# Performance work log

Measured on AMD Instinct MI355X. Metric: run time of the kernel, lower is better.

## Reference

```python
import jax, jax.numpy as jnp
import numpy as np

B, T, H, L = 8, 256, 64, 3
NB, NF, HP = 17, 68, 6
K = 9  # temporal kernel
PAD = (K - 1) // 2
EPS = 1e-5


def _normalize(adj):
    adj = adj + np.eye(adj.shape[0], dtype=np.float32)
    d = adj.sum(1)
    dinv = np.power(d, -0.5)
    dinv[np.isinf(dinv)] = 0.0
    return (dinv[:, None] * adj * dinv[None, :]).astype(np.float32)


def _body_adj():
    a = np.zeros((NB, NB), np.float32)
    conns = [(0, 1), (0, 2), (1, 3), (2, 4), (0, 5), (0, 6), (5, 6), (5, 7), (7, 9), (6, 8), (8, 10), (5, 11), (6, 12), (11, 12), (11, 13), (13, 15), (12, 14), (14, 16)]
    for i, j in conns:
        a[i, j] = 1.0
        a[j, i] = 1.0
    return _normalize(a)


def _face_adj():
    a = np.zeros((NF, NF), np.float32)
    for i in range(16): a[i, i + 1] = 1.0
    for i in range(17, 21): a[i, i + 1] = 1.0
    for i in range(22, 26): a[i, i + 1] = 1.0
    for i in range(27, 30): a[i, i + 1] = 1.0
    for i in range(31, 35): a[i, i + 1] = 1.0
    for i in range(36, 41): a[i, i + 1] = 1.0
    a[41, 36] = 1.0
    for i in range(42, 47): a[i, i + 1] = 1.0
    a[47, 42] = 1.0
    for i in range(48, 59): a[i, i + 1] = 1.0
    a[59, 48] = 1.0
    for i in range(60, 67): a[i, i + 1] = 1.0
    a[67, 60] = 1.0
    a = a + a.T
    return _normalize(a)


def setup_inputs() -> dict:
    keys = iter(jax.random.split(jax.random.key(0), 80))

    def rn(shape, s):
        return jax.random.normal(next(keys), shape, jnp.float32) * s

    inp = {}
    inp['body_kps'] = jax.random.normal(next(keys), (B, T, NB * 2), jnp.float32)
    inp['face_kps_2d'] = jax.random.normal(next(keys), (B, T, NF * 2), jnp.float32)
    inp['head_pose'] = jax.random.normal(next(keys), (B, T, HP), jnp.float32)
    inp['body_adj'] = jnp.asarray(_body_adj())
    inp['face_adj'] = jnp.asarray(_face_adj())
    inp['body_proj_w'] = rn((2, H), 0.5)
    inp['body_proj_b'] = jnp.zeros((H,), jnp.float32)
    inp['face_proj_w'] = rn((2, H), 0.5)
    inp['face_proj_b'] = jnp.zeros((H,), jnp.float32)
    inp['head_w'] = rn((HP, H), 0.3)
    inp['head_b'] = jnp.zeros((H,), jnp.float32)
    for p in ('b', 'f'):
        inp[p + '_t1w'] = rn((L, H, H, K), 0.04)
        inp[p + '_t1b'] = jnp.zeros((L, H), jnp.float32)
        inp[p + '_bn1g'] = jnp.ones((L, H), jnp.float32)
        inp[p + '_bn1b'] = jnp.zeros((L, H), jnp.float32)
        inp[p + '_bn1m'] = rn((L, H), 0.1)
        inp[p + '_bn1v'] = jax.random.uniform(next(keys), (L, H), jnp.float32, 0.5, 1.5)
        inp[p + '_gcw'] = rn((L, H, H), 0.1)
        inp[p + '_gcb'] = jnp.zeros((L, H), jnp.float32)
        inp[p + '_t2w'] = rn((L, H, H, K), 0.04)
        inp[p + '_t2b'] = jnp.zeros((L, H), jnp.float32)
        inp[p + '_bn2g'] = jnp.ones((L, H), jnp.float32)
        inp[p + '_bn2b'] = jnp.zeros((L, H), jnp.float32)
        inp[p + '_bn2m'] = rn((L, H), 0.1)
        inp[p + '_bn2v'] = jax.random.uniform(next(keys), (L, H), jnp.float32, 0.5, 1.5)
    total = NB * H + NF * H + H  # 5504
    inp['fus1_w'] = rn((total, 4 * H), 0.02)
    inp['fus1_b'] = jnp.zeros((4 * H,), jnp.float32)
    inp['fus2_w'] = rn((4 * H, 2 * H), 0.06)
    inp['fus2_b'] = jnp.zeros((2 * H,), jnp.float32)
    inp['fus3_w'] = rn((2 * H, H), 0.09)
    inp['fus3_b'] = jnp.zeros((H,), jnp.float32)
    inp['fus4_w'] = rn((H, 5), 0.12)
    inp['fus4_b'] = jnp.zeros((5,), jnp.float32)
    return inp


def _conv_bn(x, w, b, g, be, m, v):
    # x: (BN, C, T); w: (O, I, K). Conv1d (pad=4) + eval-mode BatchNorm1d.
    y = jax.lax.conv_general_dilated(x, w, (1,), [(PAD, PAD)], dimension_numbers=('NCH', 'OIH', 'NCH'))
    y = y + b[None, :, None]
    inv = g * jax.lax.rsqrt(v + EPS)
    return y * inv[None, :, None] + (be - m * inv)[None, :, None]


def _block(x, adj, t1w, t1b, g1, b1, m1, v1, gw, gb, t2w, t2b, g2, b2, m2, v2):
    # x: (B, N, C, T); residual is identity (in_channels == out_channels)
    Bn, N, C, Tn = x.shape
    res = x
    h = jax.nn.relu(_conv_bn(x.reshape(Bn * N, C, Tn), t1w, t1b, g1, b1, m1, v1)).reshape(Bn, N, C, Tn)
    # spatial graph conv, batched over all timesteps at once (adj @ (x W) + b)
    support = jnp.einsum('bnct,co->bnot', h, gw)
    h = jax.nn.relu(jnp.einsum('mn,bnot->bmot', adj, support) + gb[None, None, :, None])
    h = _conv_bn(h.reshape(Bn * N, C, Tn), t2w, t2b, g2, b2, m2, v2).reshape(Bn, N, C, Tn)
    return h + res  # dropout = identity in eval


def _stream(x, n_nodes, pw, pb, adj, ps):
    Bn, Tn, _ = x.shape
    h = x.reshape(Bn, Tn, n_nodes, 2) @ pw + pb          # (B, T, N, H)
    h = jnp.transpose(h, (0, 2, 3, 1))                   # (B, N, H, T)
    for l in range(ps[0].shape[0]):
        h = _block(h, adj, *(p[l] for p in ps))
    return h.mean(axis=3).reshape(Bn, -1)                # temporal mean-pool, flatten nodes


def reference(body_kps, face_kps_2d, head_pose, body_adj, face_adj, body_proj_w, body_proj_b, face_proj_w, face_proj_b, head_w, head_b, b_t1w, b_t1b, b_bn1g, b_bn1b, b_bn1m, b_bn1v, b_gcw, b_gcb, b_t2w, b_t2b, b_bn2g, b_bn2b, b_bn2m, b_bn2v, f_t1w, f_t1b, f_bn1g, f_bn1b, f_bn1m, f_bn1v, f_gcw, f_gcb, f_t2w, f_t2b, f_bn2g, f_bn2b, f_bn2m, f_bn2v, fus1_w, fus1_b, fus2_w, fus2_b, fus3_w, fus3_b, fus4_w, fus4_b):
    bps = (b_t1w, b_t1b, b_bn1g, b_bn1b, b_bn1m, b_bn1v, b_gcw, b_gcb, b_t2w, b_t2b, b_bn2g, b_bn2b, b_bn2m, b_bn2v)
    fps = (f_t1w, f_t1b, f_bn1g, f_bn1b, f_bn1m, f_bn1v, f_gcw, f_gcb, f_t2w, f_t2b, f_bn2g, f_bn2b, f_bn2m, f_bn2v)
    bf = _stream(body_kps, NB, body_proj_w, body_proj_b, body_adj, bps)
    ff = _stream(face_kps_2d, NF, face_proj_w, face_proj_b, face_adj, fps)
    hp = jax.nn.relu(head_pose @ head_w + head_b).mean(axis=1)
    feat = jnp.concatenate([bf, ff, hp], axis=-1)
    h = jax.nn.relu(feat @ fus1_w + fus1_b)
    h = jax.nn.relu(h @ fus2_w + fus2_b)
    h = jax.nn.relu(h @ fus3_w + fus3_b)
    return h @ fus4_w + fus4_b
```

## Files before the change

kernel.cpp:

```cpp
#include <hip/hip_runtime.h>

constexpr int B_ = 8, T_ = 256, H_ = 64, L_ = 3, NB_ = 17, NF_ = 68, HP_ = 6, K_ = 9;
constexpr int FEAT_DIM = NB_ * H_ + NF_ * H_ + H_;
constexpr int HT = H_ * T_;

typedef _Float16 half4_t __attribute__((ext_vector_type(4)));
typedef _Float16 half8_t __attribute__((ext_vector_type(8)));
typedef float f32x16 __attribute__((ext_vector_type(16)));
typedef float f32x4 __attribute__((ext_vector_type(4)));

constexpr size_t SZ_AB = (size_t)B_ * NB_ * HT;
constexpr size_t SZ_AF = (size_t)B_ * NF_ * HT;
constexpr size_t OFF_TB   = 0;
constexpr size_t OFF_TF   = OFF_TB + SZ_AB / 2;
constexpr size_t OFF_SUPB = OFF_TF + SZ_AF / 2;
constexpr size_t OFF_SUPF = OFF_SUPB + SZ_AB / 2;
constexpr size_t OFF_GB   = OFF_SUPF + SZ_AF / 2;
constexpr size_t OFF_GF   = OFF_GB + SZ_AB / 2;
constexpr size_t OFF_W3   = OFF_GF + SZ_AF / 2;
constexpr size_t OFF_GW3  = OFF_W3 + 4 * 55296;
constexpr size_t OFF_B2   = OFF_GW3 + 2 * 6144;
constexpr size_t OFF_ADJPB= OFF_B2 + 768;
constexpr size_t OFF_ADJPF= OFF_ADJPB + 512;
constexpr size_t OFF_FEAT = OFF_ADJPF + 3840;
constexpr size_t OFF_P1   = OFF_FEAT + (size_t)B_ * FEAT_DIM;

struct ConvPrepSet { const float *w, *tb, *g, *bb, *m, *v; };

struct Args {
    const float *body_kps, *face_kps, *head_pose, *body_adj, *face_adj;
    const float *body_pw, *body_pb, *face_pw, *face_pb, *head_w, *head_b;
    ConvPrepSet sb1, sb2, sf1, sf2;
    const float *b_gcw, *f_gcw, *b_gcb, *f_gcb;
    const float *fus1_w, *fus1_b, *fus2_w, *fus2_b, *fus3_w, *fus3_b, *fus4_w, *fus4_b;
    _Float16 *TrB, *TrF, *SupB, *SupF, *Gb, *Gf;
    _Float16 *W3, *GW3, *adjPB, *adjPF;
    float *B2, *p1, *feat;
    float *out;
};

__device__ __forceinline__ half8_t ld_b8(const _Float16* p) {
    half4_t lo = *(const half4_t*)p;
    half4_t hi = *(const half4_t*)(p + 4);
    return __builtin_shufflevector(lo, hi, 0, 1, 2, 3, 4, 5, 6, 7);
}

__device__ __forceinline__ void st_b8(_Float16* p, half8_t v) {
    half4_t lo, hi;
#pragma unroll
    for (int j = 0; j < 4; ++j) { lo[j] = v[j]; hi[j] = v[4 + j]; }
    *(half4_t*)p = lo;
    *(half4_t*)(p + 4) = hi;
}

__device__ __forceinline__ void stage_chunk(const _Float16* __restrict__ xb,
                                            _Float16* __restrict__ Xs, int tc, int tid) {
    for (int u = tid; u < 136 * 8; u += 256) {
        int row = u >> 3, c = u & 7;
        int t = tc * 128 + row - 4;
        half8_t v;
        if (t >= 0 && t < T_) {
            v = *(const half8_t*)(xb + (size_t)t * H_ + c * 8);
        } else {
#pragma unroll
            for (int j = 0; j < 8; ++j) v[j] = (_Float16)0.f;
        }
        st_b8(&Xs[row * 68 + c * 8], v);
    }
}

__device__ __forceinline__ void stage_res_chunk(const _Float16* __restrict__ xb,
                                                _Float16* __restrict__ Rs, int tc, int tid) {
    for (int u = tid; u < 128 * 8; u += 256) {
        int row = u >> 3, c = u & 7;
        half8_t v = *(const half8_t*)(xb + (size_t)(tc * 128 + row) * H_ + c * 8);
        st_b8(&Rs[row * 68 + c * 8], v);
    }
}

__device__ __forceinline__ void conv_kloop(const half8_t* __restrict__ wl,
                                           const _Float16* __restrict__ Xs,
                                           int trow, int ln31, int kg,
                                           f32x16 (&acc)[2]) {
    const _Float16* xr0 = Xs + (size_t)(trow + ln31) * 68;
#pragma unroll
    for (int tap = 0; tap < K_; ++tap) {
#pragma unroll
        for (int ks = 0; ks < 4; ++ks) {
            int i8 = ks * 2 + kg;
            half8_t a0 = wl[(tap * 8 + i8) * H_ + ln31];
            half8_t a1 = wl[(tap * 8 + i8) * H_ + 32 + ln31];
            half8_t bf = ld_b8(xr0 + tap * 68 + i8 * 8);
            acc[0] = __builtin_amdgcn_mfma_f32_32x32x16_f16(a0, bf, acc[0], 0, 0, 0);
            acc[1] = __builtin_amdgcn_mfma_f32_32x32x16_f16(a1, bf, acc[1], 0, 0, 0);
        }
    }
}

__device__ void convmix_core(const half8_t* __restrict__ wl,
                             const float* __restrict__ b1l,
                             const half8_t* __restrict__ gl,
                             _Float16* __restrict__ supb,
                             int tc, _Float16* __restrict__ Xs, int tid) {
    int ln = tid & 63;
    int w = __builtin_amdgcn_readfirstlane(tid >> 6);
    int ln31 = ln & 31, kg = ln >> 5;
    int trow = w * 32;

    f32x16 acc[2];
#pragma unroll
    for (int mt = 0; mt < 2; ++mt)
#pragma unroll
        for (int r = 0; r < 16; ++r) acc[mt][r] = 0.f;

    conv_kloop(wl, Xs, trow, ln31, kg, acc);
    __syncthreads();

    _Float16* mrow = Xs + (size_t)(4 + trow + ln31) * 68;
#pragma unroll
    for (int mt = 0; mt < 2; ++mt) {
#pragma unroll
        for (int rg = 0; rg < 4; ++rg) {
            int o0 = mt * 32 + rg * 8 + kg * 4;
            f32x4 bv = *(const f32x4*)(b1l + o0);
            half4_t hv;
#pragma unroll
            for (int j = 0; j < 4; ++j)
                hv[j] = (_Float16)fmaxf(acc[mt][rg * 4 + j] + bv[j], 0.f);
            *(half4_t*)(mrow + o0) = hv;
        }
    }
    __syncthreads();

    f32x16 acc2[2];
#pragma unroll
    for (int mt = 0; mt < 2; ++mt)
#pragma unroll
        for (int r = 0; r < 16; ++r) acc2[mt][r] = 0.f;
#pragma unroll
    for (int ks = 0; ks < 4; ++ks) {
        int i8 = ks * 2 + kg;
        half8_t a0 = gl[i8 * H_ + ln31];
        half8_t a1 = gl[i8 * H_ + 32 + ln31];
        half8_t b0 = ld_b8(mrow + i8 * 8);
        acc2[0] = __builtin_amdgcn_mfma_f32_32x32x16_f16(a0, b0, acc2[0], 0, 0, 0);
        acc2[1] = __builtin_amdgcn_mfma_f32_32x32x16_f16(a1, b0, acc2[1], 0, 0, 0);
    }

#pragma unroll
    for (int mt = 0; mt < 2; ++mt) {
#pragma unroll
        for (int rg = 0; rg < 4; ++rg) {
            int o0 = mt * 32 + rg * 8 + kg * 4;
            half4_t hv;
#pragma unroll
            for (int j = 0; j < 4; ++j)
                hv[j] = (_Float16)acc2[mt][rg * 4 + j];
            *(half4_t*)(mrow + o0) = hv;
        }
    }
    __syncthreads();
    _Float16* gout = supb + (size_t)(tc * 128) * H_;
    const _Float16* srow = Xs + 4 * 68;
#pragma unroll
    for (int k2 = 0; k2 < 4; ++k2) {
        int u = k2 * 256 + tid;
        int r = u >> 3, c = u & 7;
        half8_t v = ld_b8(srow + r * 68 + c * 8);
        *(half8_t*)(gout + (size_t)r * H_ + c * 8) = v;
    }
}

__global__ __launch_bounds__(256) void prep_k(Args A) {
    int blk = blockIdx.x;
    int tid = threadIdx.x;
    if (blk < 1728) {
        int set = blk / 432;
        int bx = blk % 432;
        ConvPrepSet s = (set == 0) ? A.sb1 : (set == 1) ? A.sb2 : (set == 2) ? A.sf1 : A.sf2;
        int idx = bx * 256 + tid;
        int k = idx % K_; int r = idx / K_;
        int i = r % H_; r /= H_;
        int o = r % H_; int l = r / H_;
        float sc = s.g[l * H_ + o] * rsqrtf(s.v[l * H_ + o] + 1e-5f);
        A.W3[(size_t)set * 110592 + ((((l * K_ + k) * 8 + (i >> 3)) * H_ + o) * 8) + (i & 7)]
            = (_Float16)(s.w[idx] * sc);
        if (i == 0 && k == 0)
            A.B2[set * 192 + l * H_ + o] =
                s.tb[l * H_ + o] * sc + s.bb[l * H_ + o] - s.m[l * H_ + o] * sc;
    } else if (blk < 1824) {
        int set = (blk - 1728) / 48;
        int bx = (blk - 1728) % 48;
        const float* gw = set ? A.f_gcw : A.b_gcw;
        int idx = bx * 256 + tid;
        int o = idx % H_; int r = idx / H_;
        int c = r % H_; int l = r / H_;
        A.GW3[(size_t)set * 12288 + (((l * 8 + (c >> 3)) * H_ + o) * 8) + (c & 7)]
            = (_Float16)gw[idx];
    } else {
        int idx = (blk - 1824) * 256 + tid;
        if (idx < 1024) {
            int m = idx >> 5, k = idx & 31;
            A.adjPB[idx] = (m < NB_ && k < NB_) ? (_Float16)A.body_adj[m * NB_ + k] : (_Float16)0.f;
        } else if (idx < 8704) {
            int j = idx - 1024;
            int m = j / 80, k = j % 80;
            A.adjPF[j] = (m < NF_ && k < NF_) ? (_Float16)A.face_adj[m * NF_ + k] : (_Float16)0.f;
        } else if (idx < 10752) {
            A.p1[idx - 8704] = 0.f;
        } else if (idx < 10752 + B_ * FEAT_DIM) {
            A.feat[idx - 10752] = 0.f;
        }
    }
}

__global__ __launch_bounds__(256, 4) void projcm_k(Args A) {
    __shared__ __align__(16) _Float16 Xs[136 * 68];
    int blk = blockIdx.x, tid = threadIdx.x;
    bool isB = blk < 2 * B_ * NB_;
    int j = isB ? blk : blk - 2 * B_ * NB_;
    int bn = j >> 1, tc = j & 1;
    const float* kps = isB ? A.body_kps : A.face_kps;
    const float* pw  = isB ? A.body_pw  : A.face_pw;
    const float* pb  = isB ? A.body_pb  : A.face_pb;
    _Float16* trunk  = isB ? A.TrB : A.TrF;
    int N = isB ? NB_ : NF_;
    int b = bn / N, n = bn % N;

    for (int u = tid; u < 272; u += 256) {
        int row = u >> 1, hf = u & 1;
        int t = tc * 128 + row - 4;
        _Float16* xr = Xs + row * 68 + hf * 32;
        if (t >= 0 && t < T_) {
            float x0 = kps[((size_t)b * T_ + t) * (N * 2) + n * 2 + 0];
            float x1 = kps[((size_t)b * T_ + t) * (N * 2) + n * 2 + 1];
            bool own = (row >= 4 && row < 132);
            _Float16* ob = trunk + (size_t)bn * HT + (size_t)t * H_ + hf * 32;
#pragma unroll
            for (int cg2 = 0; cg2 < 4; ++cg2) {
                half8_t v;
#pragma unroll
                for (int jj = 0; jj < 8; ++jj) {
                    int c = hf * 32 + cg2 * 8 + jj;
                    v[jj] = (_Float16)fmaf(x0, pw[c], fmaf(x1, pw[H_ + c], pb[c]));
                }
                st_b8(xr + cg2 * 8, v);
                if (own) *(half8_t*)(ob + cg2 * 8) = v;
            }
        } else {
            half8_t z;
#pragma unroll
            for (int jj = 0; jj < 8; ++jj) z[jj] = (_Float16)0.f;
            st_b8(xr, z);
            st_b8(xr + 8, z);
            st_b8(xr + 16, z);
            st_b8(xr + 24, z);
        }
    }
    __syncthreads();

    const half8_t* w1 = (const half8_t*)(A.W3 + (isB ? 0 : 221184));
    const float* b1l  = isB ? A.B2 : A.B2 + 384;
    const half8_t* gl = (const half8_t*)(A.GW3 + (isB ? 0 : 12288));
    _Float16* supb = (isB ? A.SupB : A.SupF) + (size_t)bn * HT;
    convmix_core(w1, b1l, gl, supb, tc, Xs, tid);
}

__global__ __launch_bounds__(256, 4) void cm_k(Args A, int l) {
    __shared__ __align__(16) _Float16 Xs[136 * 68];
    int blk = blockIdx.x, tid = threadIdx.x;
    bool isB = blk < 2 * B_ * NB_;
    int j = isB ? blk : blk - 2 * B_ * NB_;
    int bn = j >> 1, tc = j & 1;
    const _Float16* trunk = isB ? A.TrB : A.TrF;

    stage_chunk(trunk + (size_t)bn * HT, Xs, tc, tid);
    __syncthreads();

    const half8_t* w1 = (const half8_t*)(A.W3 + (isB ? 0 : 221184)) + (size_t)l * (K_ * 8 * H_);
    const float* b1l  = (isB ? A.B2 : A.B2 + 384) + l * H_;
    const half8_t* gl = (const half8_t*)(A.GW3 + (isB ? 0 : 12288)) + (size_t)l * (8 * H_);
    _Float16* supb = (isB ? A.SupB : A.SupF) + (size_t)bn * HT;
    convmix_core(w1, b1l, gl, supb, tc, Xs, tid);
}

template <int N, int MT, int KS>
__device__ void adjmix_impl(const _Float16* __restrict__ sup,
                            const half8_t* __restrict__ adjP,
                            const float* __restrict__ gb,
                            _Float16* __restrict__ out,
                            int blk, int l, _Float16* Ls, int tid) {
    constexpr int KP = KS * 16;
    constexpr int PITCH = KP + 4;
    int b = blk >> 7, cb = blk & 127;
    int colbase = cb * 128;

    for (int u = tid; u < KP * 16; u += 256) {
        int n = u >> 4, cs = u & 15;
        half8_t v;
        if (n < N) v = *(const half8_t*)(sup + (size_t)(b * N + n) * HT + colbase + cs * 8);
        else {
#pragma unroll
            for (int j = 0; j < 8; ++j) v[j] = (_Float16)0.f;
        }
#pragma unroll
        for (int j = 0; j < 8; ++j) Ls[(cs * 8 + j) * PITCH + n] = v[j];
    }
    __syncthreads();

    int ln = tid & 63;
    int w = __builtin_amdgcn_readfirstlane(tid >> 6);
    int ln31 = ln & 31, kg = ln >> 5;
    int colL = w * 32 + ln31;

    f32x16 acc[MT];
#pragma unroll
    for (int mt = 0; mt < MT; ++mt)
#pragma unroll
        for (int r = 0; r < 16; ++r) acc[mt][r] = 0.f;

#pragma unroll
    for (int ks = 0; ks < KS; ++ks) {
        half8_t bf = ld_b8(&Ls[colL * PITCH + ks * 16 + kg * 8]);
#pragma unroll
        for (int mt = 0; mt < MT; ++mt) {
            half8_t af = adjP[(size_t)(mt * 32 + ln31) * (KP / 8) + ks * 2 + kg];
            acc[mt] = __builtin_amdgcn_mfma_f32_32x32x16_f16(af, bf, acc[mt], 0, 0, 0);
        }
    }
    __syncthreads();

    float gbv = gb[l * H_ + (colL & 63)];
#pragma unroll
    for (int mt = 0; mt < MT; ++mt) {
#pragma unroll
        for (int r = 0; r < 16; ++r) {
            int m = mt * 32 + (r & 3) + 8 * (r >> 2) + 4 * kg;
            Ls[m * 132 + colL] = (_Float16)fmaxf(acc[mt][r] + gbv, 0.f);
        }
    }
    __syncthreads();

    for (int u = tid; u < N * 16; u += 256) {
        int m = u >> 4, c = u & 15;
        half8_t v = ld_b8(&Ls[m * 132 + c * 8]);
        *(half8_t*)(out + (size_t)(b * N + m) * HT + colbase + c * 8) = v;
    }
}

__global__ __launch_bounds__(256) void adjmix_k(Args A, int l) {
    __shared__ __align__(16) _Float16 Ls[12800];
    int blk = blockIdx.x, tid = threadIdx.x;
    if (blk < 1024)
        adjmix_impl<NB_, 1, 2>(A.SupB, (const half8_t*)A.adjPB, A.b_gcb, A.Gb, blk, l, Ls, tid);
    else
        adjmix_impl<NF_, 3, 5>(A.SupF, (const half8_t*)A.adjPF, A.f_gcb, A.Gf, blk - 1024, l, Ls, tid);
}

__global__ __launch_bounds__(256, 4) void c2_k(Args A, int l) {
    __shared__ __align__(16) _Float16 Xs[136 * 68];
    __shared__ __align__(16) _Float16 Rs[128 * 68];
    int blk = blockIdx.x, tid = threadIdx.x;
    bool isB = blk < 2 * B_ * NB_;
    int j = isB ? blk : blk - 2 * B_ * NB_;
    int bn = j >> 1, tc = j & 1;
    const _Float16* G = isB ? A.Gb : A.Gf;
    _Float16* trunk   = isB ? A.TrB : A.TrF;
    const half8_t* w2 = (const half8_t*)(A.W3 + (isB ? 110592 : 331776)) + (size_t)l * (K_ * 8 * H_);
    const float* b2l  = (isB ? A.B2 + 192 : A.B2 + 576) + l * H_;

    stage_chunk(G + (size_t)bn * HT, Xs, tc, tid);
    stage_res_chunk(trunk + (size_t)bn * HT, Rs, tc, tid);
    __syncthreads();

    int ln = tid & 63;
    int w = __builtin_amdgcn_readfirstlane(tid >> 6);
    int ln31 = ln & 31, kg = ln >> 5;
    int trow = w * 32;

    f32x16 acc[2];
#pragma unroll
    for (int mt = 0; mt < 2; ++mt)
#pragma unroll
        for (int r = 0; r < 16; ++r) acc[mt][r] = 0.f;

    conv_kloop(w2, Xs, trow, ln31, kg, acc);
    __syncthreads();

    {
        _Float16* orow = Xs + (size_t)(4 + trow + ln31) * 68;
        const _Float16* rrow = Rs + (size_t)(trow + ln31) * 68;
#pragma unroll
        for (int mt = 0; mt < 2; ++mt) {
#pragma unroll
            for (int rg = 0; rg < 4; ++rg) {
                int o0 = mt * 32 + rg * 8 + kg * 4;
                f32x4 bv = *(const f32x4*)(b2l + o0);
                half4_t rv = *(const half4_t*)(rrow + o0);
                half4_t hv;
#pragma unroll
                for (int jj = 0; jj < 4; ++jj)
                    hv[jj] = (_Float16)(acc[mt][rg * 4 + jj] + bv[jj] + (float)rv[jj]);
                *(half4_t*)(orow + o0) = hv;
            }
        }
    }
    __syncthreads();

    _Float16* gout = trunk + (size_t)bn * HT + (size_t)(tc * 128) * H_;
    const _Float16* srow = Xs + 4 * 68;
#pragma unroll
    for (int k2 = 0; k2 < 4; ++k2) {
        int u = k2 * 256 + tid;
        int r = u >> 3, c = u & 7;
        half8_t v = ld_b8(srow + r * 68 + c * 8);
        *(half8_t*)(gout + (size_t)r * H_ + c * 8) = v;
    }
}

__global__ __launch_bounds__(256, 4) void c2last_k(Args A) {
    __shared__ __align__(16) _Float16 Xs[136 * 68];
    __shared__ __align__(16) _Float16 Rs[128 * 68];
    int blk = blockIdx.x, tid = threadIdx.x;
    if (blk >= 1360) {
        int b = blk - 1360;
        if (tid < 64) {
            int c = tid;
            float w0 = A.head_w[c], w1 = A.head_w[64 + c], w2 = A.head_w[128 + c],
                  w3 = A.head_w[192 + c], w4 = A.head_w[256 + c], w5 = A.head_w[320 + c];
            float bias = A.head_b[c];
            float acc = 0.f;
            for (int t = 0; t < T_; ++t) {
                const float* xr = A.head_pose + ((size_t)b * T_ + t) * HP_;
                float s = fmaf(xr[0], w0, fmaf(xr[1], w1, fmaf(xr[2], w2,
                          fmaf(xr[3], w3, fmaf(xr[4], w4, fmaf(xr[5], w5, bias))))));
                acc += fmaxf(s, 0.f);
            }
            A.feat[(size_t)b * FEAT_DIM + NB_ * H_ + NF_ * H_ + c] = acc * (1.f / 256.f);
        }
        return;
    }
    constexpr int l = L_ - 1;
    bool isB = blk < 2 * B_ * NB_;
    int j = isB ? blk : blk - 2 * B_ * NB_;
    int bn = j >> 1, tc = j & 1;
    const _Float16* G = isB ? A.Gb : A.Gf;
    _Float16* trunk   = isB ? A.TrB : A.TrF;
    const half8_t* w2 = (const half8_t*)(A.W3 + (isB ? 110592 : 331776)) + (size_t)l * (K_ * 8 * H_);
    const float* b2l  = (isB ? A.B2 + 192 : A.B2 + 576) + l * H_;
    int N = isB ? NB_ : NF_;
    int fbase = isB ? 0 : NB_ * H_;

    stage_chunk(G + (size_t)bn * HT, Xs, tc, tid);
    stage_res_chunk(trunk + (size_t)bn * HT, Rs, tc, tid);
    __syncthreads();

    int ln = tid & 63;
    int w = __builtin_amdgcn_readfirstlane(tid >> 6);
    int ln31 = ln & 31, kg = ln >> 5;
    int trow = w * 32;

    f32x16 acc[2];
#pragma unroll
    for (int mt = 0; mt < 2; ++mt)
#pragma unroll
        for (int r = 0; r < 16; ++r) acc[mt][r] = 0.f;

    conv_kloop(w2, Xs, trow, ln31, kg, acc);

    float sv[2][16];
    const _Float16* rrow = Rs + (size_t)(trow + ln31) * 68;
#pragma unroll
    for (int mt = 0; mt < 2; ++mt) {
#pragma unroll
        for (int rg = 0; rg < 4; ++rg) {
            int o0 = mt * 32 + rg * 8 + kg * 4;
            f32x4 bv = *(const f32x4*)(b2l + o0);
            half4_t rv = *(const half4_t*)(rrow + o0);
#pragma unroll
            for (int jj = 0; jj < 4; ++jj) {
                int r = rg * 4 + jj;
                float s = acc[mt][r] + bv[jj] + (float)rv[jj];
#pragma unroll
                for (int off = 1; off < 32; off <<= 1) s += __shfl_xor(s, off);
                sv[mt][r] = s;
            }
        }
    }
    __syncthreads();
    float* red = (float*)Xs;
    if (ln31 == 0) {
#pragma unroll
        for (int mt = 0; mt < 2; ++mt)
#pragma unroll
            for (int r = 0; r < 16; ++r) {
                int o = mt * 32 + (r & 3) + 8 * (r >> 2) + 4 * kg;
                red[w * 64 + o] = sv[mt][r];
            }
    }
    __syncthreads();
    if (tid < 64) {
        float s = red[tid] + red[64 + tid] + red[128 + tid] + red[192 + tid];
        int b = bn / N, n = bn % N;
        atomicAdd(&A.feat[(size_t)b * FEAT_DIM + fbase + n * H_ + tid], s * (1.f / 256.f));
    }
}

__global__ __launch_bounds__(256) void fus1_k(Args A) {
    __shared__ float fv[8][64];
    int blk = blockIdx.x;
    int ic = blk >> 1, kh = blk & 1;
    int base = ic * 128 + kh * 64;
    int tid = threadIdx.x;
    for (int u = tid; u < 8 * 64; u += 256) {
        int b = u >> 6, j = u & 63;
        fv[b][j] = A.feat[(size_t)b * FEAT_DIM + base + j];
    }
    __syncthreads();
    float acc[8];
#pragma unroll
    for (int b = 0; b < 8; ++b) acc[b] = 0.f;
    const float* wb = A.fus1_w + (size_t)base * 256 + tid;
    for (int i = 0; i < 64; ++i) {
        float wv = wb[(size_t)i * 256];
#pragma unroll
        for (int b = 0; b < 8; ++b) acc[b] = fmaf(fv[b][i], wv, acc[b]);
    }
#pragma unroll
    for (int b = 0; b < 8; ++b) atomicAdd(&A.p1[b * 256 + tid], acc[b]);
}

__global__ __launch_bounds__(256) void fus_tail_k(Args A) {
    __shared__ float s1[256], s2[128], s3[64];
    int b = blockIdx.x, tid = threadIdx.x;
    s1[tid] = fmaxf(A.p1[b * 256 + tid] + A.fus1_b[tid], 0.f);
    __syncthreads();
    if (tid < 128) {
        float acc = A.fus2_b[tid];
        for (int i = 0; i < 256; ++i) acc = fmaf(s1[i], A.fus2_w[i * 128 + tid], acc);
        s2[tid] = fmaxf(acc, 0.f);
    }
    __syncthreads();
    if (tid < 64) {
        float acc = A.fus3_b[tid];
        for (int i = 0; i < 128; ++i) acc = fmaf(s2[i], A.fus3_w[i * 64 + tid], acc);
        s3[tid] = fmaxf(acc, 0.f);
    }
    __syncthreads();
    if (tid < 5) {
        float acc = A.fus4_b[tid];
        for (int i = 0; i < 64; ++i) acc = fmaf(s3[i], A.fus4_w[i * 5 + tid], acc);
        A.out[b * 5 + tid] = acc;
    }
}

extern "C" void kernel_launch(void* const* d_in, const int* in_sizes, int n_in,
                              void* d_out, int out_size, void* d_ws, size_t ws_size,
                              hipStream_t stream) {
    float* ws = (float*)d_ws;

    Args A;
    A.body_kps = (const float*)d_in[0];
    A.face_kps = (const float*)d_in[1];
    A.head_pose = (const float*)d_in[2];
    A.body_adj = (const float*)d_in[3];
    A.face_adj = (const float*)d_in[4];
    A.body_pw = (const float*)d_in[5];
    A.body_pb = (const float*)d_in[6];
    A.face_pw = (const float*)d_in[7];
    A.face_pb = (const float*)d_in[8];
    A.head_w = (const float*)d_in[9];
    A.head_b = (const float*)d_in[10];
    A.sb1 = ConvPrepSet{(const float*)d_in[11], (const float*)d_in[12], (const float*)d_in[13],
                        (const float*)d_in[14], (const float*)d_in[15], (const float*)d_in[16]};
    A.b_gcw = (const float*)d_in[17];
    A.b_gcb = (const float*)d_in[18];
    A.sb2 = ConvPrepSet{(const float*)d_in[19], (const float*)d_in[20], (const float*)d_in[21],
                        (const float*)d_in[22], (const float*)d_in[23], (const float*)d_in[24]};
    A.sf1 = ConvPrepSet{(const float*)d_in[25], (const float*)d_in[26], (const float*)d_in[27],
                        (const float*)d_in[28], (const float*)d_in[29], (const float*)d_in[30]};
    A.f_gcw = (const float*)d_in[31];
    A.f_gcb = (const float*)d_in[32];
    A.sf2 = ConvPrepSet{(const float*)d_in[33], (const float*)d_in[34], (const float*)d_in[35],
                        (const float*)d_in[36], (const float*)d_in[37], (const float*)d_in[38]};
    A.fus1_w = (const float*)d_in[39]; A.fus1_b = (const float*)d_in[40];
    A.fus2_w = (const float*)d_in[41]; A.fus2_b = (const float*)d_in[42];
    A.fus3_w = (const float*)d_in[43]; A.fus3_b = (const float*)d_in[44];
    A.fus4_w = (const float*)d_in[45]; A.fus4_b = (const float*)d_in[46];

    A.TrB  = (_Float16*)(ws + OFF_TB);
    A.TrF  = (_Float16*)(ws + OFF_TF);
    A.SupB = (_Float16*)(ws + OFF_SUPB);
    A.SupF = (_Float16*)(ws + OFF_SUPF);
    A.Gb   = (_Float16*)(ws + OFF_GB);
    A.Gf   = (_Float16*)(ws + OFF_GF);
    A.W3   = (_Float16*)(ws + OFF_W3);
    A.GW3  = (_Float16*)(ws + OFF_GW3);
    A.adjPB= (_Float16*)(ws + OFF_ADJPB);
    A.adjPF= (_Float16*)(ws + OFF_ADJPF);
    A.B2   = ws + OFF_B2;
    A.feat = ws + OFF_FEAT;
    A.p1   = ws + OFF_P1;
    A.out  = (float*)d_out;

    prep_k<<<2038, 256, 0, stream>>>(A);
    projcm_k<<<1360, 256, 0, stream>>>(A);
    for (int l = 0; l < L_; ++l) {
        adjmix_k<<<2048, 256, 0, stream>>>(A, l);
        if (l < L_ - 1) {
            c2_k<<<1360, 256, 0, stream>>>(A, l);
            cm_k<<<1360, 256, 0, stream>>>(A, l + 1);
        } else {
            c2last_k<<<1368, 256, 0, stream>>>(A);
        }
    }
    fus1_k<<<86, 256, 0, stream>>>(A);
    fus_tail_k<<<8, 256, 0, stream>>>(A);
}
```

Measured before the change: 382.9 us.

## Halve temporal tile to 64 rows and split waves across output-channel halves

The conv kernels now process 64-timestep chunks instead of 128, giving four chunks per node sequence and twice as many blocks. Each wave computes one 32x32 output tile, split as 2 time-slices by 2 output-channel halves, instead of two output tiles over 32 timesteps. Shared memory per block shrinks, and the launch bounds request 8 blocks per CU instead of 4, to raise occupancy and balance the grid. The cost is more halo recomputation (8 of 72 rows instead of 8 of 136), more block overhead, and twice as many atomicAdds into the pooled features.

After: 372.8 us (median of 2 runs). 1.03x faster.

```diff
diff --git a/kernel.cpp b/kernel.cpp
--- a/kernel.cpp
+++ b/kernel.cpp
@@ -53,11 +53,11 @@
     *(half4_t*)(p + 4) = hi;
 }
 
-__device__ __forceinline__ void stage_chunk(const _Float16* __restrict__ xb,
-                                            _Float16* __restrict__ Xs, int tc, int tid) {
-    for (int u = tid; u < 136 * 8; u += 256) {
+__device__ __forceinline__ void stage_chunk64(const _Float16* __restrict__ xb,
+                                              _Float16* __restrict__ Xs, int tc, int tid) {
+    for (int u = tid; u < 72 * 8; u += 256) {
         int row = u >> 3, c = u & 7;
-        int t = tc * 128 + row - 4;
+        int t = tc * 64 + row - 4;
         half8_t v;
         if (t >= 0 && t < T_) {
             v = *(const half8_t*)(xb + (size_t)t * H_ + c * 8);
@@ -69,30 +69,28 @@
     }
 }
 
-__device__ __forceinline__ void stage_res_chunk(const _Float16* __restrict__ xb,
-                                                _Float16* __restrict__ Rs, int tc, int tid) {
-    for (int u = tid; u < 128 * 8; u += 256) {
+__device__ __forceinline__ void stage_res64(const _Float16* __restrict__ xb,
+                                            _Float16* __restrict__ Rs, int tc, int tid) {
+    for (int u = tid; u < 64 * 8; u += 256) {
         int row = u >> 3, c = u & 7;
-        half8_t v = *(const half8_t*)(xb + (size_t)(tc * 128 + row) * H_ + c * 8);
+        half8_t v = *(const half8_t*)(xb + (size_t)(tc * 64 + row) * H_ + c * 8);
         st_b8(&Rs[row * 68 + c * 8], v);
     }
 }
 
 __device__ __forceinline__ void conv_kloop(const half8_t* __restrict__ wl,
                                            const _Float16* __restrict__ Xs,
-                                           int trow, int ln31, int kg,
-                                           f32x16 (&acc)[2]) {
+                                           int trow, int ln31, int kg, int ot,
+                                           f32x16& acc) {
     const _Float16* xr0 = Xs + (size_t)(trow + ln31) * 68;
 #pragma unroll
     for (int tap = 0; tap < K_; ++tap) {
 #pragma unroll
         for (int ks = 0; ks < 4; ++ks) {
             int i8 = ks * 2 + kg;
-            half8_t a0 = wl[(tap * 8 + i8) * H_ + ln31];
-            half8_t a1 = wl[(tap * 8 + i8) * H_ + 32 + ln31];
+            half8_t a = wl[(tap * 8 + i8) * H_ + ot * 32 + ln31];
             half8_t bf = ld_b8(xr0 + tap * 68 + i8 * 8);
-            acc[0] = __builtin_amdgcn_mfma_f32_32x32x16_f16(a0, bf, acc[0], 0, 0, 0);
-            acc[1] = __builtin_amdgcn_mfma_f32_32x32x16_f16(a1, bf, acc[1], 0, 0, 0);
+            acc = __builtin_amdgcn_mfma_f32_32x32x16_f16(a, bf, acc, 0, 0, 0);
         }
     }
 }
@@ -105,65 +103,55 @@
     int ln = tid & 63;
     int w = __builtin_amdgcn_readfirstlane(tid >> 6);
     int ln31 = ln & 31, kg = ln >> 5;
-    int trow = w * 32;
-
-    f32x16 acc[2];
-#pragma unroll
-    for (int mt = 0; mt < 2; ++mt)
-#pragma unroll
-        for (int r = 0; r < 16; ++r) acc[mt][r] = 0.f;
-
-    conv_kloop(wl, Xs, trow, ln31, kg, acc);
+    int ts = w & 1, ot = w >> 1;
+    int trow = ts * 32;
+
+    f32x16 acc;
+#pragma unroll
+    for (int r = 0; r < 16; ++r) acc[r] = 0.f;
+
+    conv_kloop(wl, Xs, trow, ln31, kg, ot, acc);
     __syncthreads();
 
     _Float16* mrow = Xs + (size_t)(4 + trow + ln31) * 68;
 #pragma unroll
-    for (int mt = 0; mt < 2; ++mt) {
-#pragma unroll
-        for (int rg = 0; rg < 4; ++rg) {
-            int o0 = mt * 32 + rg * 8 + kg * 4;
-            f32x4 bv = *(const f32x4*)(b1l + o0);
-            half4_t hv;
-#pragma unroll
-            for (int j = 0; j < 4; ++j)
-                hv[j] = (_Float16)fmaxf(acc[mt][rg * 4 + j] + bv[j], 0.f);
-            *(half4_t*)(mrow + o0) = hv;
-        }
-    }
-    __syncthreads();
-
-    f32x16 acc2[2];
-#pragma unroll
-    for (int mt = 0; mt < 2; ++mt)
-#pragma unroll
-        for (int r = 0; r < 16; ++r) acc2[mt][r] = 0.f;
+    for (int rg = 0; rg < 4; ++rg) {
+        int o0 = ot * 32 + rg * 8 + kg * 4;
+        f32x4 bv = *(const f32x4*)(b1l + o0);
+        half4_t hv;
+#pragma unroll
+        for (int j = 0; j < 4; ++j)
+            hv[j] = (_Float16)fmaxf(acc[rg * 4 + j] + bv[j], 0.f);
+        *(half4_t*)(mrow + o0) = hv;
+    }
+    __syncthreads();
+
+    f32x16 acc2;
+#pragma unroll
+    for (int r = 0; r < 16; ++r) acc2[r] = 0.f;
 #pragma unroll
     for (int ks = 0; ks < 4; ++ks) {
         int i8 = ks * 2 + kg;
-        half8_t a0 = gl[i8 * H_ + ln31];
-        half8_t a1 = gl[i8 * H_ + 32 + ln31];
-        half8_t b0 = ld_b8(mrow + i8 * 8);
-        acc2[0] = __builtin_amdgcn_mfma_f32_32x32x16_f16(a0, b0, acc2[0], 0, 0, 0);
-        acc2[1] = __builtin_amdgcn_mfma_f32_32x32x16_f16(a1, b0, acc2[1], 0, 0, 0);
-    }
-
-#pragma unroll
-    for (int mt = 0; mt < 2; ++mt) {
-#pragma unroll
-        for (int rg = 0; rg < 4; ++rg) {
-            int o0 = mt * 32 + rg * 8 + kg * 4;
-            half4_t hv;
-#pragma unroll
-            for (int j = 0; j < 4; ++j)
-                hv[j] = (_Float16)acc2[mt][rg * 4 + j];
-            *(half4_t*)(mrow + o0) = hv;
-        }
-    }
-    __syncthreads();
-    _Float16* gout = supb + (size_t)(tc * 128) * H_;
+        half8_t a = gl[i8 * H_ + ot * 32 + ln31];
+        half8_t bf = ld_b8(mrow + i8 * 8);
+        acc2 = __builtin_amdgcn_mfma_f32_32x32x16_f16(a, bf, acc2, 0, 0, 0);
+    }
+    __syncthreads();
+
+#pragma unroll
+    for (int rg = 0; rg < 4; ++rg) {
+        int o0 = ot * 32 + rg * 8 + kg * 4;
+        half4_t hv;
+#pragma unroll
+        for (int j = 0; j < 4; ++j)
+            hv[j] = (_Float16)acc2[rg * 4 + j];
+        *(half4_t*)(mrow + o0) = hv;
+    }
+    __syncthreads();
+    _Float16* gout = supb + (size_t)(tc * 64) * H_;
     const _Float16* srow = Xs + 4 * 68;
 #pragma unroll
-    for (int k2 = 0; k2 < 4; ++k2) {
+    for (int k2 = 0; k2 < 2; ++k2) {
         int u = k2 * 256 + tid;
         int r = u >> 3, c = u & 7;
         half8_t v = ld_b8(srow + r * 68 + c * 8);
@@ -214,12 +202,12 @@
     }
 }
 
-__global__ __launch_bounds__(256, 4) void projcm_k(Args A) {
-    __shared__ __align__(16) _Float16 Xs[136 * 68];
+__global__ __launch_bounds__(256, 8) void projcm_k(Args A) {
+    __shared__ __align__(16) _Float16 Xs[72 * 68];
     int blk = blockIdx.x, tid = threadIdx.x;
-    bool isB = blk < 2 * B_ * NB_;
-    int j = isB ? blk : blk - 2 * B_ * NB_;
-    int bn = j >> 1, tc = j & 1;
+    bool isB = blk < 4 * B_ * NB_;
+    int j = isB ? blk : blk - 4 * B_ * NB_;
+    int bn = j >> 2, tc = j & 3;
     const float* kps = isB ? A.body_kps : A.face_kps;
     const float* pw  = isB ? A.body_pw  : A.face_pw;
     const float* pb  = isB ? A.body_pb  : A.face_pb;
@@ -227,14 +215,14 @@
     int N = isB ? NB_ : NF_;
     int b = bn / N, n = bn % N;
 
-    for (int u = tid; u < 272; u += 256) {
-        int row = u >> 1, hf = u & 1;
-        int t = tc * 128 + row - 4;
+    if (tid < 144) {
+        int row = tid >> 1, hf = tid & 1;
+        int t = tc * 64 + row - 4;
         _Float16* xr = Xs + row * 68 + hf * 32;
         if (t >= 0 && t < T_) {
             float x0 = kps[((size_t)b * T_ + t) * (N * 2) + n * 2 + 0];
             float x1 = kps[((size_t)b * T_ + t) * (N * 2) + n * 2 + 1];
-            bool own = (row >= 4 && row < 132);
+            bool own = (row >= 4 && row < 68);
             _Float16* ob = trunk + (size_t)bn * HT + (size_t)t * H_ + hf * 32;
 #pragma unroll
             for (int cg2 = 0; cg2 < 4; ++cg2) {
@@ -266,15 +254,15 @@
     convmix_core(w1, b1l, gl, supb, tc, Xs, tid);
 }
 
-__global__ __launch_bounds__(256, 4) void cm_k(Args A, int l) {
-    __shared__ __align__(16) _Float16 Xs[136 * 68];
+__global__ __launch_bounds__(256, 8) void cm_k(Args A, int l) {
+    __shared__ __align__(16) _Float16 Xs[72 * 68];
     int blk = blockIdx.x, tid = threadIdx.x;
-    bool isB = blk < 2 * B_ * NB_;
-    int j = isB ? blk : blk - 2 * B_ * NB_;
-    int bn = j >> 1, tc = j & 1;
+    bool isB = blk < 4 * B_ * NB_;
+    int j = isB ? blk : blk - 4 * B_ * NB_;
+    int bn = j >> 2, tc = j & 3;
     const _Float16* trunk = isB ? A.TrB : A.TrF;
 
-    stage_chunk(trunk + (size_t)bn * HT, Xs, tc, tid);
+    stage_chunk64(trunk + (size_t)bn * HT, Xs, tc, tid);
     __syncthreads();
 
     const half8_t* w1 = (const half8_t*)(A.W3 + (isB ? 0 : 221184)) + (size_t)l * (K_ * 8 * H_);
@@ -357,60 +345,56 @@
         adjmix_impl<NF_, 3, 5>(A.SupF, (const half8_t*)A.adjPF, A.f_gcb, A.Gf, blk - 1024, l, Ls, tid);
 }
 
-__global__ __launch_bounds__(256, 4) void c2_k(Args A, int l) {
-    __shared__ __align__(16) _Float16 Xs[136 * 68];
-    __shared__ __align__(16) _Float16 Rs[128 * 68];
+__global__ __launch_bounds__(256, 8) void c2_k(Args A, int l) {
+    __shared__ __align__(16) _Float16 Xs[72 * 68];
+    __shared__ __align__(16) _Float16 Rs[64 * 68];
     int blk = blockIdx.x, tid = threadIdx.x;
-    bool isB = blk < 2 * B_ * NB_;
-    int j = isB ? blk : blk - 2 * B_ * NB_;
-    int bn = j >> 1, tc = j & 1;
+    bool isB = blk < 4 * B_ * NB_;
+    int j = isB ? blk : blk - 4 * B_ * NB_;
+    int bn = j >> 2, tc = j & 3;
     const _Float16* G = isB ? A.Gb : A.Gf;
     _Float16* trunk   = isB ? A.TrB : A.TrF;
     const half8_t* w2 = (const half8_t*)(A.W3 + (isB ? 110592 : 331776)) + (size_t)l * (K_ * 8 * H_);
     const float* b2l  = (isB ? A.B2 + 192 : A.B2 + 576) + l * H_;
 
-    stage_chunk(G + (size_t)bn * HT, Xs, tc, tid);
-    stage_res_chunk(trunk + (size_t)bn * HT, Rs, tc, tid);
+    stage_chunk64(G + (size_t)bn * HT, Xs, tc, tid);
+    stage_res64(trunk + (size_t)bn * HT, Rs, tc, tid);
     __syncthreads();
 
     int ln = tid & 63;
     int w = __builtin_amdgcn_readfirstlane(tid >> 6);
     int ln31 = ln & 31, kg = ln >> 5;
-    int trow = w * 32;
-
-    f32x16 acc[2];
-#pragma unroll
-    for (int mt = 0; mt < 2; ++mt)
-#pragma unroll
-        for (int r = 0; r < 16; ++r) acc[mt][r] = 0.f;
-
-    conv_kloop(w2, Xs, trow, ln31, kg, acc);
+    int ts = w & 1, ot = w >> 1;
+    int trow = ts * 32;
+
+    f32x16 acc;
+#pragma unroll
+    for (int r = 0; r < 16; ++r) acc[r] = 0.f;
+
+    conv_kloop(w2, Xs, trow, ln31, kg, ot, acc);
     __syncthreads();
 
     {
         _Float16* orow = Xs + (size_t)(4 + trow + ln31) * 68;
         const _Float16* rrow = Rs + (size_t)(trow + ln31) * 68;
 #pragma unroll
-        for (int mt = 0; mt < 2; ++mt) {
-#pragma unroll
-            for (int rg = 0; rg < 4; ++rg) {
-                int o0 = mt * 32 + rg * 8 + kg * 4;
-                f32x4 bv = *(const f32x4*)(b2l + o0);
-                half4_t rv = *(const half4_t*)(rrow + o0);
-                half4_t hv;
-#pragma unroll
-                for (int jj = 0; jj < 4; ++jj)
-                    hv[jj] = (_Float16)(acc[mt][rg * 4 + jj] + bv[jj] + (float)rv[jj]);
-                *(half4_t*)(orow + o0) = hv;
-            }
-        }
-    }
-    __syncthreads();
-
-    _Float16* gout = trunk + (size_t)bn * HT + (size_t)(tc * 128) * H_;
+        for (int rg = 0; rg < 4; ++rg) {
+            int o0 = ot * 32 + rg * 8 + kg * 4;
+            f32x4 bv = *(const f32x4*)(b2l + o0);
+            half4_t rv = *(const half4_t*)(rrow + o0);
+            half4_t hv;
+#pragma unroll
+            for (int jj = 0; jj < 4; ++jj)
+                hv[jj] = (_Float16)(acc[rg * 4 + jj] + bv[jj] + (float)rv[jj]);
+            *(half4_t*)(orow + o0) = hv;
+        }
+    }
+    __syncthreads();
+
+    _Float16* gout = trunk + (size_t)bn * HT + (size_t)(tc * 64) * H_;
     const _Float16* srow = Xs + 4 * 68;
 #pragma unroll
-    for (int k2 = 0; k2 < 4; ++k2) {
+    for (int k2 = 0; k2 < 2; ++k2) {
         int u = k2 * 256 + tid;
         int r = u >> 3, c = u & 7;
         half8_t v = ld_b8(srow + r * 68 + c * 8);
@@ -418,12 +402,12 @@
     }
 }
 
-__global__ __launch_bounds__(256, 4) void c2last_k(Args A) {
-    __shared__ __align__(16) _Float16 Xs[136 * 68];
-    __shared__ __align__(16) _Float16 Rs[128 * 68];
+__global__ __launch_bounds__(256, 8) void c2last_k(Args A) {
+    __shared__ __align__(16) _Float16 Xs[72 * 68];
+    __shared__ __align__(16) _Float16 Rs[64 * 68];
     int blk = blockIdx.x, tid = threadIdx.x;
-    if (blk >= 1360) {
-        int b = blk - 1360;
+    if (blk >= 2720) {
+        int b = blk - 2720;
         if (tid < 64) {
             int c = tid;
             float w0 = A.head_w[c], w1 = A.head_w[64 + c], w2 = A.head_w[128 + c],
@@ -441,9 +425,9 @@
         return;
     }
     constexpr int l = L_ - 1;
-    bool isB = blk < 2 * B_ * NB_;
-    int j = isB ? blk : blk - 2 * B_ * NB_;
-    int bn = j >> 1, tc = j & 1;
+    bool isB = blk < 4 * B_ * NB_;
+    int j = isB ? blk : blk - 4 * B_ * NB_;
+    int bn = j >> 2, tc = j & 3;
     const _Float16* G = isB ? A.Gb : A.Gf;
     _Float16* trunk   = isB ? A.TrB : A.TrF;
     const half8_t* w2 = (const half8_t*)(A.W3 + (isB ? 110592 : 331776)) + (size_t)l * (K_ * 8 * H_);
@@ -451,58 +435,53 @@
     int N = isB ? NB_ : NF_;
     int fbase = isB ? 0 : NB_ * H_;
 
-    stage_chunk(G + (size_t)bn * HT, Xs, tc, tid);
-    stage_res_chunk(trunk + (size_t)bn * HT, Rs, tc, tid);
+    stage_chunk64(G + (size_t)bn * HT, Xs, tc, tid);
+    stage_res64(trunk + (size_t)bn * HT, Rs, tc, tid);
     __syncthreads();
 
     int ln = tid & 63;
     int w = __builtin_amdgcn_readfirstlane(tid >> 6);
     int ln31 = ln & 31, kg = ln >> 5;
-    int trow = w * 32;
-
-    f32x16 acc[2];
-#pragma unroll
-    for (int mt = 0; mt < 2; ++mt)
-#pragma unroll
-        for (int r = 0; r < 16; ++r) acc[mt][r] = 0.f;
-
-    conv_kloop(w2, Xs, trow, ln31, kg, acc);
-
-    float sv[2][16];
+    int ts = w & 1, ot = w >> 1;
+    int trow = ts * 32;
+
+    f32x16 acc;
+#pragma unroll
+    for (int r = 0; r < 16; ++r) acc[r] = 0.f;
+
+    conv_kloop(w2, Xs, trow, ln31, kg, ot, acc);
+
+    float sv[16];
     const _Float16* rrow = Rs + (size_t)(trow + ln31) * 68;
 #pragma unroll
-    for (int mt = 0; mt < 2; ++mt) {
-#pragma unroll
-        for (int rg = 0; rg < 4; ++rg) {
-            int o0 = mt * 32 + rg * 8 + kg * 4;
-            f32x4 bv = *(const f32x4*)(b2l + o0);
-            half4_t rv = *(const half4_t*)(rrow + o0);
-#pragma unroll
-            for (int jj = 0; jj < 4; ++jj) {
-                int r = rg * 4 + jj;
-                float s = acc[mt][r] + bv[jj] + (float)rv[jj];
-#pragma unroll
-                for (int off = 1; off < 32; off <<= 1) s += __shfl_xor(s, off);
-                sv[mt][r] = s;
-            }
+    for (int rg = 0; rg < 4; ++rg) {
+        int o0 = ot * 32 + rg * 8 + kg * 4;
+        f32x4 bv = *(const f32x4*)(b2l + o0);
+        half4_t rv = *(const half4_t*)(rrow + o0);
+#pragma unroll
+        for (int jj = 0; jj < 4; ++jj) {
+            int r = rg * 4 + jj;
+            float s = acc[r] + bv[jj] + (float)rv[jj];
+#pragma unroll
+            for (int off = 1; off < 32; off <<= 1) s += __shfl_xor(s, off);
+            sv[r] = s;
         }
     }
     __syncthreads();
     float* red = (float*)Xs;
     if (ln31 == 0) {
 #pragma unroll
-        for (int mt = 0; mt < 2; ++mt)
-#pragma unroll
-            for (int r = 0; r < 16; ++r) {
-                int o = mt * 32 + (r & 3) + 8 * (r >> 2) + 4 * kg;
-                red[w * 64 + o] = sv[mt][r];
-            }
+        for (int r = 0; r < 16; ++r) {
+            int olocal = (r & 3) + 8 * (r >> 2) + 4 * kg;
+            red[w * 32 + olocal] = sv[r];
+        }
     }
     __syncthreads();
     if (tid < 64) {
-        float s = red[tid] + red[64 + tid] + red[128 + tid] + red[192 + tid];
+        int o = tid, ot2 = o >> 5, ol = o & 31;
+        float s = red[(ot2 * 2) * 32 + ol] + red[(ot2 * 2 + 1) * 32 + ol];
         int b = bn / N, n = bn % N;
-        atomicAdd(&A.feat[(size_t)b * FEAT_DIM + fbase + n * H_ + tid], s * (1.f / 256.f));
+        atomicAdd(&A.feat[(size_t)b * FEAT_DIM + fbase + n * H_ + o], s * (1.f / 256.f));
     }
 }
 
@@ -603,15 +582,17 @@
     A.p1   = ws + OFF_P1;
     A.out  = (float*)d_out;
 
+    const int gconv = 4 * (B_ * NB_ + B_ * NF_);
+
     prep_k<<<2038, 256, 0, stream>>>(A);
-    projcm_k<<<1360, 256, 0, stream>>>(A);
+    projcm_k<<<gconv, 256, 0, stream>>>(A);
     for (int l = 0; l < L_; ++l) {
         adjmix_k<<<2048, 256, 0, stream>>>(A, l);
         if (l < L_ - 1) {
-            c2_k<<<1360, 256, 0, stream>>>(A, l);
-            cm_k<<<1360, 256, 0, stream>>>(A, l + 1);
+            c2_k<<<gconv, 256, 0, stream>>>(A, l);
+            cm_k<<<gconv, 256, 0, stream>>>(A, l + 1);
         } else {
-            c2last_k<<<1368, 256, 0, stream>>>(A);
+            c2last_k<<<gconv + 8, 256, 0, stream>>>(A);
         }
     }
     fus1_k<<<86, 256, 0, stream>>>(A);
```
